# Optimization experiments

Measured on AMD Instinct MI355X. Metric: run time of the kernel, lower is better.

The kernel has to match this reference:

```python
import jax, jax.numpy as jnp
import numpy as np

NEG_SLOPE = 0.2  # PyG GATConv default


def gat_layer(x, src, dst, W, a_src, a_dst, b, num_nodes):
    """Single-head GATConv (heads=1, add_self_loops handled by caller)."""
    xw = x @ W  # [N, H]
    s_src = xw @ a_src  # [N] per-node source attention logits
    s_dst = xw @ a_dst  # [N]
    e = jax.nn.leaky_relu(s_src[src] + s_dst[dst], NEG_SLOPE)  # [E]
    # segment softmax over incoming edges of each dst node
    m = jax.ops.segment_max(e, dst, num_segments=num_nodes)  # [N]
    ex = jnp.exp(e - m[dst])
    denom = jax.ops.segment_sum(ex, dst, num_segments=num_nodes)  # [N]
    alpha = ex / denom[dst]  # [E]
    out = jax.ops.segment_sum(alpha[:, None] * xw[src], dst, num_segments=num_nodes)
    return out + b


def setup_inputs() -> dict:
    key = jax.random.key(0)
    N, F_IN, H, E, B = 100000, 256, 64, 1000000, 16384
    ks = jax.random.split(key, 16)
    s = lambda fan: 1.0 / np.sqrt(fan)
    return {
        "x": jax.random.normal(ks[0], (N, F_IN), dtype=jnp.float32),
        "edge_index": jax.random.randint(ks[1], (2, E), 0, N, dtype=jnp.int64),
        "user_indices": jax.random.randint(ks[2], (B,), 0, N, dtype=jnp.int64),
        "movie_indices": jax.random.randint(ks[3], (B,), 0, N, dtype=jnp.int64),
        "W1": jax.random.normal(ks[4], (F_IN, H), dtype=jnp.float32) * s(F_IN),
        "a_src1": jax.random.normal(ks[5], (H,), dtype=jnp.float32) * s(H),
        "a_dst1": jax.random.normal(ks[6], (H,), dtype=jnp.float32) * s(H),
        "b1": jnp.zeros((H,), dtype=jnp.float32),
        "W2": jax.random.normal(ks[7], (H, H), dtype=jnp.float32) * s(H),
        "a_src2": jax.random.normal(ks[8], (H,), dtype=jnp.float32) * s(H),
        "a_dst2": jax.random.normal(ks[9], (H,), dtype=jnp.float32) * s(H),
        "b2": jnp.zeros((H,), dtype=jnp.float32),
        "fc_W": jax.random.normal(ks[10], (2 * H, 1), dtype=jnp.float32) * s(2 * H),
        "fc_b": jnp.zeros((1,), dtype=jnp.float32),
    }


def reference(x, edge_index, user_indices, movie_indices,
              W1, a_src1, a_dst1, b1, W2, a_src2, a_dst2, b2, fc_W, fc_b):
    N = x.shape[0]
    # PyG GATConv default add_self_loops=True: append (i, i) edges
    loops = jnp.arange(N, dtype=edge_index.dtype)
    src = jnp.concatenate([edge_index[0], loops])
    dst = jnp.concatenate([edge_index[1], loops])
    h = gat_layer(x, src, dst, W1, a_src1, a_dst1, b1, N)
    h = jax.nn.relu(h)
    h = gat_layer(h, src, dst, W2, a_src2, a_dst2, b2, N)
    combined = jnp.concatenate([h[user_indices], h[movie_indices]], axis=1)  # [B, 2H]
    return combined @ fc_W + fc_b  # [B, 1]
```

## Files before the change

### kernel.cpp

```cpp
#include <hip/hip_runtime.h>
#include <hip/hip_bf16.h>
#include <hip/hip_fp16.h>

#define LRELU_SLOPE 0.2f
#define CSR_STRIDE 32

__device__ __forceinline__ float lrelu(float x) { return x > 0.f ? x : LRELU_SLOPE * x; }

typedef __attribute__((ext_vector_type(8))) short short8;
typedef __attribute__((ext_vector_type(4))) float f32x4;

__device__ __forceinline__ unsigned short f2bf(float f) {
    unsigned u = __builtin_bit_cast(unsigned, f);
    u = (u + 0x7FFFu + ((u >> 16) & 1u)) >> 16;
    return (unsigned short)u;
}
__device__ __forceinline__ float bf2f(unsigned short b) {
    unsigned u = ((unsigned)b) << 16;
    return __builtin_bit_cast(float, u);
}

template <int K>
__device__ __forceinline__ void packW_body(const float* __restrict__ W,
                                           unsigned short* __restrict__ Bhi,
                                           unsigned short* __restrict__ Blo,
                                           int blk, int t) {
    constexpr int NKC = K / 32;
    int g = blk * 256 + t;
    if (g >= 4 * NKC * 64) return;
    int lane = g & 63;
    int kc = (g >> 6) % NKC;
    int ct = g / (64 * NKC);
    int qd = lane >> 4, col = lane & 15;
    #pragma unroll
    for (int j = 0; j < 8; j++) {
        int k = kc * 32 + qd * 8 + j;
        float w = W[(size_t)k * 64 + ct * 16 + col];
        unsigned short h = f2bf(w);
        float rem = w - bf2f(h);
        Bhi[(size_t)g * 8 + j] = h;
        Blo[(size_t)g * 8 + j] = f2bf(rem);
    }
}

__global__ __launch_bounds__(256) void k_prep(const float* __restrict__ W1,
                                              unsigned short* __restrict__ b1hi, unsigned short* __restrict__ b1lo,
                                              const float* __restrict__ W2,
                                              unsigned short* __restrict__ b2hi, unsigned short* __restrict__ b2lo,
                                              int* __restrict__ csr, int* __restrict__ ovfCnt,
                                              float* __restrict__ out, const float* __restrict__ fcb,
                                              int N, int B) {
    int b = blockIdx.x;
    if (b < 8)  { packW_body<256>(W1, b1hi, b1lo, b, threadIdx.x); return; }
    if (b < 10) { packW_body<64>(W2, b2hi, b2lo, b - 8, threadIdx.x); return; }
    int i = (b - 10) * 256 + threadIdx.x;
    if (i < N) csr[(size_t)i * CSR_STRIDE] = 0;
    if (i < B) out[i] = fcb[0];
    if (i == 0) *ovfCnt = 0;
}

__global__ void k_build(const int* __restrict__ src, const int* __restrict__ dst,
                        int* __restrict__ csr,
                        int* __restrict__ ovfCnt, int2* __restrict__ ovf, int E) {
    int i = (blockIdx.x * blockDim.x + threadIdx.x) * 4;
    if (i + 3 < E) {
        int4 d4 = *(const int4*)(dst + i);
        int4 s4 = *(const int4*)(src + i);
        int p0 = atomicAdd(&csr[(size_t)d4.x * CSR_STRIDE], 1);
        int p1 = atomicAdd(&csr[(size_t)d4.y * CSR_STRIDE], 1);
        int p2 = atomicAdd(&csr[(size_t)d4.z * CSR_STRIDE], 1);
        int p3 = atomicAdd(&csr[(size_t)d4.w * CSR_STRIDE], 1);
        if (p0 < CSR_STRIDE - 1) csr[(size_t)d4.x * CSR_STRIDE + 1 + p0] = s4.x;
        else { int o = atomicAdd(ovfCnt, 1); ovf[o] = make_int2(d4.x, s4.x); }
        if (p1 < CSR_STRIDE - 1) csr[(size_t)d4.y * CSR_STRIDE + 1 + p1] = s4.y;
        else { int o = atomicAdd(ovfCnt, 1); ovf[o] = make_int2(d4.y, s4.y); }
        if (p2 < CSR_STRIDE - 1) csr[(size_t)d4.z * CSR_STRIDE + 1 + p2] = s4.z;
        else { int o = atomicAdd(ovfCnt, 1); ovf[o] = make_int2(d4.z, s4.z); }
        if (p3 < CSR_STRIDE - 1) csr[(size_t)d4.w * CSR_STRIDE + 1 + p3] = s4.w;
        else { int o = atomicAdd(ovfCnt, 1); ovf[o] = make_int2(d4.w, s4.w); }
    } else {
        for (int j = i; j < E; j++) {
            int d = dst[j], s = src[j];
            int p = atomicAdd(&csr[(size_t)d * CSR_STRIDE], 1);
            if (p < CSR_STRIDE - 1) csr[(size_t)d * CSR_STRIDE + 1 + p] = s;
            else { int o = atomicAdd(ovfCnt, 1); ovf[o] = make_int2(d, s); }
        }
    }
}

template <int K>
__device__ __forceinline__ void mfma_body(const float* __restrict__ X,
                                          const unsigned short* __restrict__ Bhi,
                                          const unsigned short* __restrict__ Blo,
                                          const float* __restrict__ a_s, const float* __restrict__ a_d,
                                          __half* __restrict__ XW, float* __restrict__ Ssrc,
                                          float* __restrict__ Sdst, int N, int blk) {
    constexpr int NKC = K / 32;
    int t = threadIdx.x, lane = t & 63, wid = t >> 6;
    int mtile = blk * 4 + wid;
    if (mtile * 16 >= N) return;
    int m0 = mtile * 16;
    int qd = lane >> 4, col = lane & 15;

    int rA = m0 + col;
    rA = rA < N ? rA : N - 1;
    const float* xrow = X + (size_t)rA * K + qd * 8;

    const short8* bh = (const short8*)Bhi;
    const short8* bl = (const short8*)Blo;

    f32x4 acc[4];
    #pragma unroll
    for (int ct = 0; ct < 4; ct++) acc[ct] = (f32x4){0.f, 0.f, 0.f, 0.f};

    #pragma clang loop unroll(disable)
    for (int kc = 0; kc < NKC; kc++) {
        const float* xp = xrow + kc * 32;
        float4 xa = *(const float4*)xp;
        float4 xb = *(const float4*)(xp + 4);
        float xv[8] = {xa.x, xa.y, xa.z, xa.w, xb.x, xb.y, xb.z, xb.w};
        short8 ah, al;
        #pragma unroll
        for (int j = 0; j < 8; j++) {
            unsigned short h = f2bf(xv[j]);
            ah[j] = (short)h;
            al[j] = (short)f2bf(xv[j] - bf2f(h));
        }
        #pragma unroll
        for (int ct = 0; ct < 4; ct++) {
            short8 wh = bh[(ct * NKC + kc) * 64 + lane];
            short8 wl = bl[(ct * NKC + kc) * 64 + lane];
            acc[ct] = __builtin_amdgcn_mfma_f32_16x16x32_bf16(ah, wh, acc[ct], 0, 0, 0);
            acc[ct] = __builtin_amdgcn_mfma_f32_16x16x32_bf16(al, wh, acc[ct], 0, 0, 0);
            acc[ct] = __builtin_amdgcn_mfma_f32_16x16x32_bf16(ah, wl, acc[ct], 0, 0, 0);
        }
    }

    float asx[4], adx[4];
    #pragma unroll
    for (int ct = 0; ct < 4; ct++) {
        asx[ct] = a_s[ct * 16 + col];
        adx[ct] = a_d[ct * 16 + col];
    }
    #pragma unroll
    for (int r = 0; r < 4; r++) {
        int row = m0 + qd * 4 + r;
        if (row < N) {
            float vs = 0.f, vd = 0.f;
            #pragma unroll
            for (int ct = 0; ct < 4; ct++) {
                float v = acc[ct][r];
                XW[(size_t)row * 64 + ct * 16 + col] = __float2half(v);
                vs += v * asx[ct];
                vd += v * adx[ct];
            }
            #pragma unroll
            for (int d = 1; d < 16; d <<= 1) {
                vs += __shfl_xor(vs, d);
                vd += __shfl_xor(vd, d);
            }
            if (col == 0) { Ssrc[row] = vs; Sdst[row] = vd; }
        }
    }
}

template <int K>
__global__ __launch_bounds__(256) void k_mfma(const float* __restrict__ X,
                                              const unsigned short* __restrict__ Bhi,
                                              const unsigned short* __restrict__ Blo,
                                              const float* __restrict__ a_s, const float* __restrict__ a_d,
                                              __half* __restrict__ XW, float* __restrict__ Ssrc,
                                              float* __restrict__ Sdst, int N) {
    mfma_body<K>(X, Bhi, Blo, a_s, a_d, XW, Ssrc, Sdst, N, blockIdx.x);
}

__global__ __launch_bounds__(256) void k_attn(const __half* __restrict__ XW, const float* __restrict__ Ssrc,
                                              const float* __restrict__ Sdst, const int* __restrict__ csr,
                                              const int* __restrict__ ovfCnt, const int2* __restrict__ ovf,
                                              const int* __restrict__ uiL, const int* __restrict__ miL, int Bn,
                                              const float* __restrict__ bias, float* __restrict__ H,
                                              const float* __restrict__ fcW, float* __restrict__ out,
                                              int N, int do_relu) {
    int t = threadIdx.x, lane = t & 63, wid = t >> 6;
    int q = lane >> 4;
    int c = lane & 15;
    int i4 = (blockIdx.x * 4 + wid) * 4 + q;
    bool valid;
    int n;
    if (uiL) {
        valid = i4 < 2 * Bn;
        n = valid ? (i4 < Bn ? uiL[i4] : miL[i4 - Bn]) : 0;
    } else {
        valid = i4 < N;
        n = valid ? i4 : 0;
    }
    int nc = n;

    int st = nc * CSR_STRIDE;
    int d = csr[st];
    float sd = Sdst[nc];
    int d31 = d < CSR_STRIDE - 1 ? d : CSR_STRIDE - 1;
    int dcap = d < 16 ? d : 16;

    int myS = 0;
    if (c < dcap) myS = csr[st + 1 + c];

    int s0 = __shfl(myS, q * 16 + 0), s1 = __shfl(myS, q * 16 + 1);
    int s2 = __shfl(myS, q * 16 + 2), s3 = __shfl(myS, q * 16 + 3);
    float2 rs = *(const float2*)(XW + (size_t)nc * 64 + c * 4);
    float2 r0 = *(const float2*)(XW + (size_t)s0 * 64 + c * 4);
    float2 r1 = *(const float2*)(XW + (size_t)s1 * 64 + c * 4);
    float2 r2 = *(const float2*)(XW + (size_t)s2 * 64 + c * 4);
    float2 r3 = *(const float2*)(XW + (size_t)s3 * 64 + c * 4);

    float wself = __expf(lrelu(Ssrc[nc] + sd));
    float myW = 0.f;
    if (c < dcap) myW = __expf(lrelu(Ssrc[myS] + sd));
    float dpart = myW + ((c == 0) ? wself : 0.f);

    float4 acc4 = make_float4(0.f, 0.f, 0.f, 0.f);
    auto accum = [&](float2 raw, float w) {
        const __half2* hp = (const __half2*)&raw;
        float2 f0 = __half22float2(hp[0]);
        float2 f1 = __half22float2(hp[1]);
        acc4.x += w * f0.x; acc4.y += w * f0.y; acc4.z += w * f1.x; acc4.w += w * f1.y;
    };

    float w0 = __shfl(myW, q * 16 + 0), w1 = __shfl(myW, q * 16 + 1);
    float w2 = __shfl(myW, q * 16 + 2), w3 = __shfl(myW, q * 16 + 3);
    accum(rs, wself);
    accum(r0, w0); accum(r1, w1); accum(r2, w2); accum(r3, w3);

    for (int i = 4; i < dcap; i += 4) {
        int t0 = __shfl(myS, q * 16 + i + 0), t1 = __shfl(myS, q * 16 + i + 1);
        int t2 = __shfl(myS, q * 16 + i + 2), t3 = __shfl(myS, q * 16 + i + 3);
        float2 q0 = *(const float2*)(XW + (size_t)t0 * 64 + c * 4);
        float2 q1 = *(const float2*)(XW + (size_t)t1 * 64 + c * 4);
        float2 q2 = *(const float2*)(XW + (size_t)t2 * 64 + c * 4);
        float2 q3 = *(const float2*)(XW + (size_t)t3 * 64 + c * 4);
        float v0 = __shfl(myW, q * 16 + i + 0), v1 = __shfl(myW, q * 16 + i + 1);
        float v2 = __shfl(myW, q * 16 + i + 2), v3 = __shfl(myW, q * 16 + i + 3);
        accum(q0, v0); accum(q1, v1); accum(q2, v2); accum(q3, v3);
    }

    for (int i = 16; i < d31; i++) {
        int s = csr[st + 1 + i];
        float w = __expf(lrelu(Ssrc[s] + sd));
        if (c == 0) dpart += w;
        float2 qv = *(const float2*)(XW + (size_t)s * 64 + c * 4);
        accum(qv, w);
    }

    int nov = *ovfCnt;
    if (nov > 0) {
        for (int j = 0; j < nov; j++) {
            int2 e = ovf[j];
            if (e.x == nc) {
                float w = __expf(lrelu(Ssrc[e.y] + sd));
                if (c == 0) dpart += w;
                float2 qv = *(const float2*)(XW + (size_t)e.y * 64 + c * 4);
                accum(qv, w);
            }
        }
    }

    #pragma unroll
    for (int dd = 8; dd > 0; dd >>= 1) dpart += __shfl_xor(dpart, dd);

    if (valid) {
        float4 b4 = *(const float4*)&bias[c * 4];
        float inv = 1.f / dpart;
        float4 o;
        o.x = acc4.x * inv + b4.x;
        o.y = acc4.y * inv + b4.y;
        o.z = acc4.z * inv + b4.z;
        o.w = acc4.w * inv + b4.w;
        if (do_relu) {
            o.x = fmaxf(o.x, 0.f); o.y = fmaxf(o.y, 0.f);
            o.z = fmaxf(o.z, 0.f); o.w = fmaxf(o.w, 0.f);
        }
        if (!uiL) {
            *(float4*)&H[(size_t)n * 64 + c * 4] = o;
        } else {
            const float* fw = fcW + (i4 < Bn ? 0 : 64) + c * 4;
            float dot = o.x * fw[0] + o.y * fw[1] + o.z * fw[2] + o.w * fw[3];
            #pragma unroll
            for (int dd = 8; dd > 0; dd >>= 1) dot += __shfl_xor(dot, dd);
            if (c == 0) atomicAdd(&out[i4 < Bn ? i4 : i4 - Bn], dot);
        }
    }
}

extern "C" void kernel_launch(void* const* d_in, const int* in_sizes, int n_in,
                              void* d_out, int out_size, void* d_ws, size_t ws_size,
                              hipStream_t stream) {
    const float* x   = (const float*)d_in[0];
    const int*   ei  = (const int*)d_in[1];
    const int*   ui  = (const int*)d_in[2];
    const int*   mi  = (const int*)d_in[3];
    const float* W1  = (const float*)d_in[4];
    const float* as1 = (const float*)d_in[5];
    const float* ad1 = (const float*)d_in[6];
    const float* b1  = (const float*)d_in[7];
    const float* W2  = (const float*)d_in[8];
    const float* as2 = (const float*)d_in[9];
    const float* ad2 = (const float*)d_in[10];
    const float* b2  = (const float*)d_in[11];
    const float* fcW = (const float*)d_in[12];
    const float* fcb = (const float*)d_in[13];
    float* out = (float*)d_out;

    const int Hdim = in_sizes[5];
    const int FIN  = in_sizes[4] / Hdim;
    const int N    = in_sizes[0] / FIN;
    const int E    = in_sizes[1] / 2;
    const int B    = in_sizes[2];

    char* w = (char*)d_ws;
    auto alloc = [&](size_t bytes) -> void* {
        void* p = (void*)w;
        w += (bytes + 255) & ~(size_t)255;
        return p;
    };
    __half* xw  = (__half*)alloc((size_t)N * 64 * 2);
    float* hbuf = (float*)alloc((size_t)N * 64 * 4);
    float* ssrc = (float*)alloc((size_t)N * 4);
    float* sdst = (float*)alloc((size_t)N * 4);
    int* csr    = (int*)alloc((size_t)N * CSR_STRIDE * 4);
    int* ovfCnt = (int*)alloc(256);
    int2* ovf   = (int2*)alloc((size_t)65536 * 8);
    unsigned short* b1hi = (unsigned short*)alloc((size_t)4 * 8 * 64 * 8 * 2);
    unsigned short* b1lo = (unsigned short*)alloc((size_t)4 * 8 * 64 * 8 * 2);
    unsigned short* b2hi = (unsigned short*)alloc((size_t)4 * 2 * 64 * 8 * 2);
    unsigned short* b2lo = (unsigned short*)alloc((size_t)4 * 2 * 64 * 8 * 2);

    const int* esrc = ei;
    const int* edst = ei + E;

    const int mfmaBlocks = ((N + 15) / 16 + 3) / 4;
    const int attnBlocks = (N + 15) / 16;
    const int attn2Blocks = (2 * B + 15) / 16;

    int prepBlocks = 10 + (N + 255) / 256;
    k_prep<<<prepBlocks, 256, 0, stream>>>(W1, b1hi, b1lo, W2, b2hi, b2lo, csr, ovfCnt, out, fcb, N, B);

    k_build<<<(E / 4 + 255) / 256, 256, 0, stream>>>(esrc, edst, csr, ovfCnt, ovf, E);

    k_mfma<256><<<mfmaBlocks, 256, 0, stream>>>(x, b1hi, b1lo, as1, ad1, xw, ssrc, sdst, N);
    k_attn<<<attnBlocks, 256, 0, stream>>>(xw, ssrc, sdst, csr, ovfCnt, ovf,
                                           (const int*)nullptr, (const int*)nullptr, 0,
                                           b1, hbuf, (const float*)nullptr, (float*)nullptr, N, 1);

    k_mfma<64><<<mfmaBlocks, 256, 0, stream>>>(hbuf, b2hi, b2lo, as2, ad2, xw, ssrc, sdst, N);
    k_attn<<<attn2Blocks, 256, 0, stream>>>(xw, ssrc, sdst, csr, ovfCnt, ovf,
                                            ui, mi, B, b2, hbuf, fcW, out, N, 0);
}
```

Before: 303.5 us.

## Split MFMA K-loop across wave pairs with LDS reduction

Each 16-row tile of the projection GEMM is now handled by two waves that each take half the K dimension, and the partial accumulators are combined through shared memory before the epilogue. The block count doubles so twice as many waves work on the latency-bound per-tile loop, shortening the serial dependency chain of MFMAs and load-convert steps. The cost is an LDS write/read and a block-wide barrier, plus half the waves sitting idle during the epilogue. For K=64, each half runs only a single K chunk.

```diff
diff --git a/kernel.cpp b/kernel.cpp
--- a/kernel.cpp
+++ b/kernel.cpp
@@ -89,22 +89,27 @@
 }
 
 template <int K>
-__device__ __forceinline__ void mfma_body(const float* __restrict__ X,
-                                          const unsigned short* __restrict__ Bhi,
-                                          const unsigned short* __restrict__ Blo,
-                                          const float* __restrict__ a_s, const float* __restrict__ a_d,
-                                          __half* __restrict__ XW, float* __restrict__ Ssrc,
-                                          float* __restrict__ Sdst, int N, int blk) {
+__global__ __launch_bounds__(256) void k_mfma(const float* __restrict__ X,
+                                              const unsigned short* __restrict__ Bhi,
+                                              const unsigned short* __restrict__ Blo,
+                                              const float* __restrict__ a_s, const float* __restrict__ a_d,
+                                              __half* __restrict__ XW, float* __restrict__ Ssrc,
+                                              float* __restrict__ Sdst, int N) {
     constexpr int NKC = K / 32;
+    constexpr int NKH = NKC / 2;
+    __shared__ f32x4 red[2][4][64];
+
     int t = threadIdx.x, lane = t & 63, wid = t >> 6;
-    int mtile = blk * 4 + wid;
-    if (mtile * 16 >= N) return;
-    int m0 = mtile * 16;
+    int pair = wid >> 1, half = wid & 1;
+    int mtile = blockIdx.x * 2 + pair;
+    int maxt = (N + 15) / 16 - 1;
+    int mt = mtile < maxt ? mtile : maxt;
+    int m0 = mt * 16;
     int qd = lane >> 4, col = lane & 15;
 
     int rA = m0 + col;
     rA = rA < N ? rA : N - 1;
-    const float* xrow = X + (size_t)rA * K + qd * 8;
+    const float* xrow = X + (size_t)rA * K + half * (NKH * 32) + qd * 8;
 
     const short8* bh = (const short8*)Bhi;
     const short8* bl = (const short8*)Blo;
@@ -114,7 +119,7 @@
     for (int ct = 0; ct < 4; ct++) acc[ct] = (f32x4){0.f, 0.f, 0.f, 0.f};
 
     #pragma clang loop unroll(disable)
-    for (int kc = 0; kc < NKC; kc++) {
+    for (int kc = 0; kc < NKH; kc++) {
         const float* xp = xrow + kc * 32;
         float4 xa = *(const float4*)xp;
         float4 xb = *(const float4*)(xp + 4);
@@ -126,15 +131,26 @@
             ah[j] = (short)h;
             al[j] = (short)f2bf(xv[j] - bf2f(h));
         }
+        int kcg = half * NKH + kc;
         #pragma unroll
         for (int ct = 0; ct < 4; ct++) {
-            short8 wh = bh[(ct * NKC + kc) * 64 + lane];
-            short8 wl = bl[(ct * NKC + kc) * 64 + lane];
+            short8 wh = bh[(ct * NKC + kcg) * 64 + lane];
+            short8 wl = bl[(ct * NKC + kcg) * 64 + lane];
             acc[ct] = __builtin_amdgcn_mfma_f32_16x16x32_bf16(ah, wh, acc[ct], 0, 0, 0);
             acc[ct] = __builtin_amdgcn_mfma_f32_16x16x32_bf16(al, wh, acc[ct], 0, 0, 0);
             acc[ct] = __builtin_amdgcn_mfma_f32_16x16x32_bf16(ah, wl, acc[ct], 0, 0, 0);
         }
     }
+
+    if (half == 1) {
+        #pragma unroll
+        for (int ct = 0; ct < 4; ct++) red[pair][ct][lane] = acc[ct];
+    }
+    __syncthreads();
+    if (half == 1) return;
+
+    #pragma unroll
+    for (int ct = 0; ct < 4; ct++) acc[ct] += red[pair][ct][lane];
 
     float asx[4], adx[4];
     #pragma unroll
@@ -162,16 +178,6 @@
             if (col == 0) { Ssrc[row] = vs; Sdst[row] = vd; }
         }
     }
-}
-
-template <int K>
-__global__ __launch_bounds__(256) void k_mfma(const float* __restrict__ X,
-                                              const unsigned short* __restrict__ Bhi,
-                                              const unsigned short* __restrict__ Blo,
-                                              const float* __restrict__ a_s, const float* __restrict__ a_d,
-                                              __half* __restrict__ XW, float* __restrict__ Ssrc,
-                                              float* __restrict__ Sdst, int N) {
-    mfma_body<K>(X, Bhi, Blo, a_s, a_d, XW, Ssrc, Sdst, N, blockIdx.x);
 }
 
 __global__ __launch_bounds__(256) void k_attn(const __half* __restrict__ XW, const float* __restrict__ Ssrc,
@@ -337,7 +343,7 @@
     const int* esrc = ei;
     const int* edst = ei + E;
 
-    const int mfmaBlocks = ((N + 15) / 16 + 3) / 4;
+    const int mfmaBlocks = (((N + 15) / 16) + 1) / 2;
     const int attnBlocks = (N + 15) / 16;
     const int attn2Blocks = (2 * B + 15) / 16;
 
```

Result: no change. 301.5 us (-0.7%).
